# Performance work log

Measured on AMD Instinct MI355X. Metric: run time of the kernel, lower is better.

Reference implementation:

```python
import jax, jax.numpy as jnp
import numpy as np
from jax import lax

H = 20  # hidden_size


def _rnn_layer(x_seq, h0, W_ih, W_hh, b_ih, b_hh):
    """Vanilla tanh RNN layer. x_seq: [B,T,D], h0: [B,H]. Returns ([B,T,H], [B,H])."""
    # Precompute input projection for all timesteps (the only large GEMM).
    xp = jnp.einsum('btd,hd->bth', x_seq, W_ih) + b_ih + b_hh  # [B,T,H]

    def step(h, xt):
        h = jnp.tanh(xt + h @ W_hh.T)
        return h, h

    h_last, hs = lax.scan(step, h0, jnp.swapaxes(xp, 0, 1))  # hs: [T,B,H]
    return jnp.swapaxes(hs, 0, 1), h_last


def setup_inputs() -> dict:
    key = jax.random.key(0)
    ks = jax.random.split(key, 12)
    B, T = 4096, 512
    s = 1.0 / np.sqrt(H)  # PyTorch default uniform(-1/sqrt(H), 1/sqrt(H))
    u = lambda k, shape: jax.random.uniform(k, shape, jnp.float32, -s, s)
    return {
        'x': jax.random.normal(ks[0], (B, T, 1), jnp.float32),
        'hidden': jax.random.normal(ks[1], (2, B, H), jnp.float32),
        'W_ih0': u(ks[2], (H, 1)),
        'W_hh0': u(ks[3], (H, H)),
        'b_ih0': u(ks[4], (H,)),
        'b_hh0': u(ks[5], (H,)),
        'W_ih1': u(ks[6], (H, H)),
        'W_hh1': u(ks[7], (H, H)),
        'b_ih1': u(ks[8], (H,)),
        'b_hh1': u(ks[9], (H,)),
        'fc_w': u(ks[10], (1, H)),
        'fc_b': u(ks[11], (1,)),
    }


def reference(x, hidden, W_ih0, W_hh0, b_ih0, b_hh0, W_ih1, W_hh1, b_ih1, b_hh1, fc_w, fc_b):
    # 2-layer vanilla RNN (eval mode: inter-layer dropout disabled)
    h0_seq, h0_last = _rnn_layer(x, hidden[0], W_ih0, W_hh0, b_ih0, b_hh0)
    h1_seq, h1_last = _rnn_layer(h0_seq, hidden[1], W_ih1, W_hh1, b_ih1, b_hh1)
    out = h1_seq[:, -1, :] @ fc_w.T + fc_b  # [B,1]
    new_hidden = jnp.stack([h0_last, h1_last], axis=0)  # [2,B,H]
    return out, new_hidden
```

## Files before the change

### kernel.cpp

```cpp
#include <hip/hip_runtime.h>


#define Bsz 4096
#define Tn  512
#define Hn  20
#define GB  3
#define XPAD 520
#define NTHREADS 128

typedef float v2 __attribute__((ext_vector_type(2)));

__device__ __forceinline__ float tanh_fast(float v) {
    float e = __expf(2.0f * v);
    return 1.0f - 2.0f * __builtin_amdgcn_rcpf(e + 1.0f);
}

#define DOT20P(acc, accb, W, H) do { \
    acc  = __builtin_elementwise_fma(W##0, H##0, acc);  \
    accb = __builtin_elementwise_fma(W##1, H##1, accb); \
    acc  = __builtin_elementwise_fma(W##2, H##2, acc);  \
    accb = __builtin_elementwise_fma(W##3, H##3, accb); \
    acc  = __builtin_elementwise_fma(W##4, H##4, acc);  \
    accb = __builtin_elementwise_fma(W##5, H##5, accb); \
    acc  = __builtin_elementwise_fma(W##6, H##6, acc);  \
    accb = __builtin_elementwise_fma(W##7, H##7, accb); \
    acc  = __builtin_elementwise_fma(W##8, H##8, acc);  \
    accb = __builtin_elementwise_fma(W##9, H##9, accb); \
} while (0)

#define LOAD_ROWP(W, ptr) \
    v2 W##0, W##1, W##2, W##3, W##4, W##5, W##6, W##7, W##8, W##9; \
    { const float4* _p = (const float4*)(ptr); \
      float4 _t; \
      _t = _p[0]; W##0 = (v2){_t.x, _t.y}; W##1 = (v2){_t.z, _t.w}; \
      _t = _p[1]; W##2 = (v2){_t.x, _t.y}; W##3 = (v2){_t.z, _t.w}; \
      _t = _p[2]; W##4 = (v2){_t.x, _t.y}; W##5 = (v2){_t.z, _t.w}; \
      _t = _p[3]; W##6 = (v2){_t.x, _t.y}; W##7 = (v2){_t.z, _t.w}; \
      _t = _p[4]; W##8 = (v2){_t.x, _t.y}; W##9 = (v2){_t.z, _t.w}; }

#define READ_H(H, base) \
    v2 H##0, H##1, H##2, H##3, H##4, H##5, H##6, H##7, H##8, H##9; \
    { const float4 _a = *(const float4*)((base) + 0);  \
      const float4 _b = *(const float4*)((base) + 4);  \
      const float4 _c = *(const float4*)((base) + 8);  \
      const float4 _d = *(const float4*)((base) + 12); \
      const float4 _e = *(const float4*)((base) + 16); \
      H##0 = (v2){_a.x, _a.y}; H##1 = (v2){_a.z, _a.w}; \
      H##2 = (v2){_b.x, _b.y}; H##3 = (v2){_b.z, _b.w}; \
      H##4 = (v2){_c.x, _c.y}; H##5 = (v2){_c.z, _c.w}; \
      H##6 = (v2){_d.x, _d.y}; H##7 = (v2){_d.z, _d.w}; \
      H##8 = (v2){_e.x, _e.y}; H##9 = (v2){_e.z, _e.w}; }

__global__ __launch_bounds__(NTHREADS)
__attribute__((amdgpu_waves_per_eu(1, 4)))
void rnn2_fused(const float* __restrict__ x,
                const float* __restrict__ hidden,
                const float* __restrict__ W_ih0,
                const float* __restrict__ W_hh0,
                const float* __restrict__ b_ih0,
                const float* __restrict__ b_hh0,
                const float* __restrict__ W_ih1,
                const float* __restrict__ W_hh1,
                const float* __restrict__ b_ih1,
                const float* __restrict__ b_hh1,
                const float* __restrict__ fc_w,
                const float* __restrict__ fc_b,
                float* __restrict__ out)
{
    const int tid  = threadIdx.x;
    const int wave = tid >> 6;
    const int lane = tid & 63;
    int g = lane / Hn;
    int j = lane - g * Hn;
    const bool lane_ok = (lane < GB * Hn);
    if (!lane_ok) { g = GB - 1; j = lane - 60; }

    const int  b        = blockIdx.x * GB + g;
    const bool b_ok     = (b < Bsz);
    const int  bl       = b_ok ? b : (Bsz - 1);
    const bool store_ok = lane_ok && b_ok;

    __shared__ float xs[GB][XPAD];
    __shared__ float h0s[2][GB][Hn];
    __shared__ float h1s[GB][Hn];

    const float* rowA = (wave == 0) ? (W_hh0 + j * Hn) : (W_ih1 + j * Hn);
    LOAD_ROWP(wA, rowA)
    LOAD_ROWP(wB, W_hh1 + j * Hn)

    const float wih0  = W_ih0[j];
    const float bias0 = b_ih0[j] + b_hh0[j];
    const float bias1 = b_ih1[j] + b_hh1[j];

    {
        const int bB = blockIdx.x * GB;
        #pragma unroll
        for (int r = 0; r < (GB * Tn) / (NTHREADS * 4); ++r) {
            const int c  = (r * NTHREADS + tid) * 4;
            const int gg = c >> 9;
            const int t  = c & (Tn - 1);
            const int bb = (bB + gg < Bsz) ? (bB + gg) : (Bsz - 1);
            float4 v = *(const float4*)(x + (long)bb * Tn + t);
            *(float4*)&xs[gg][t] = v;
        }
    }

    if (wave == 0) h0s[1][g][j] = hidden[bl * Hn + j];
    else           h1s[g][j]    = hidden[(long)Bsz * Hn + bl * Hn + j];
    __syncthreads();

    float n_keep = 0.f;

    #pragma unroll 2
    for (int i = 0; i < Tn; ++i) {
        const int p = (i + 1) & 1, q = i & 1;
        if (wave == 0) {
            READ_H(hA, &h0s[p][g][0])
            const float xt = xs[g][i];
            v2 a  = (v2){fmaf(xt, wih0, bias0), 0.f};
            v2 ab = (v2){0.f, 0.f};
            DOT20P(a, ab, wA, hA);
            const v2 s = a + ab;
            const float n = tanh_fast(s.x + s.y);
            h0s[q][g][j] = n;
            n_keep = n;
        } else if (i > 0) {
            READ_H(hA, &h0s[p][g][0])
            READ_H(hB, &h1s[g][0])
            v2 a1  = (v2){bias1, 0.f};
            v2 a1b = (v2){0.f, 0.f};
            v2 a2  = (v2){0.f, 0.f};
            v2 a2b = (v2){0.f, 0.f};
            DOT20P(a1, a1b, wA, hA);
            DOT20P(a2, a2b, wB, hB);
            const v2 s = (a1 + a1b) + (a2 + a2b);
            const float n = tanh_fast(s.x + s.y);
            h1s[g][j] = n;
            n_keep = n;
        }
        __syncthreads();
    }

    if (wave == 0) {
        if (store_ok)
            out[Bsz + (long)b * Hn + j] = n_keep;
    } else {
        READ_H(hA, &h0s[1][g][0])
        READ_H(hB, &h1s[g][0])
        v2 a1  = (v2){bias1, 0.f};
        v2 a1b = (v2){0.f, 0.f};
        v2 a2  = (v2){0.f, 0.f};
        v2 a2b = (v2){0.f, 0.f};
        DOT20P(a1, a1b, wA, hA);
        DOT20P(a2, a2b, wB, hB);
        const v2 s = (a1 + a1b) + (a2 + a2b);
        const float n1_last = tanh_fast(s.x + s.y);
        h1s[g][j] = n1_last;

        if (store_ok) {
            out[Bsz + (long)Bsz * Hn + (long)b * Hn + j] = n1_last;
            if (j == 0) {
                LOAD_ROWP(fw, fc_w)
                READ_H(hv, &h1s[g][0])
                v2 aA = (v2){fc_b[0], 0.f};
                v2 aB = (v2){0.f, 0.f};
                DOT20P(aA, aB, fw, hv);
                const v2 sf = aA + aB;
                out[b] = sf.x + sf.y;
            }
        }
    }
}

extern "C" void kernel_launch(void* const* d_in, const int* in_sizes, int n_in,
                              void* d_out, int out_size, void* d_ws, size_t ws_size,
                              hipStream_t stream) {
    const float* x      = (const float*)d_in[0];
    const float* hidden = (const float*)d_in[1];
    const float* W_ih0  = (const float*)d_in[2];
    const float* W_hh0  = (const float*)d_in[3];
    const float* b_ih0  = (const float*)d_in[4];
    const float* b_hh0  = (const float*)d_in[5];
    const float* W_ih1  = (const float*)d_in[6];
    const float* W_hh1  = (const float*)d_in[7];
    const float* b_ih1  = (const float*)d_in[8];
    const float* b_hh1  = (const float*)d_in[9];
    const float* fc_w   = (const float*)d_in[10];
    const float* fc_b   = (const float*)d_in[11];

    const int nblocks = (Bsz + GB - 1) / GB;
    rnn2_fused<<<nblocks, NTHREADS, 0, stream>>>(
        x, hidden, W_ih0, W_hh0, b_ih0, b_hh0,
        W_ih1, W_hh1, b_ih1, b_hh1, fc_w, fc_b, (float*)d_out);
}
```

Measured before the change: 133.5 us.

## Pipeline RNN layers across waves with a ring buffer and fewer barriers

Replaces the per-timestep block barrier with phases of 8 timesteps. Wave 0 (layer 0) writes its hidden states into a 16-slot shared ring, and wave 1 (layer 1) runs one phase behind, reading the half of the ring that is already finished. Within each phase, each wave relies on in-wave LDS ordering for its own recurrence, which cuts block-wide barriers from one per step to one per phase. The cost is one extra phase of pipeline latency, a larger shared-memory ring, and reliance on intra-wavefront ordering of LDS accesses.

```diff
diff --git a/kernel.cpp b/kernel.cpp
--- a/kernel.cpp
+++ b/kernel.cpp
@@ -5,6 +5,9 @@
 #define Tn  512
 #define Hn  20
 #define GB  3
+#define K   8
+#define RING 16
+#define NPH (Tn / K)
 #define XPAD 520
 #define NTHREADS 128
 
@@ -81,7 +84,7 @@
     const bool store_ok = lane_ok && b_ok;
 
     __shared__ float xs[GB][XPAD];
-    __shared__ float h0s[2][GB][Hn];
+    __shared__ float h0r[RING][GB][Hn];
     __shared__ float h1s[GB][Hn];
 
     const float* rowA = (wave == 0) ? (W_hh0 + j * Hn) : (W_ih1 + j * Hn);
@@ -105,60 +108,58 @@
         }
     }
 
-    if (wave == 0) h0s[1][g][j] = hidden[bl * Hn + j];
-    else           h1s[g][j]    = hidden[(long)Bsz * Hn + bl * Hn + j];
+    if (wave == 0) h0r[RING - 1][g][j] = hidden[bl * Hn + j];
+    else           h1s[g][j]           = hidden[(long)Bsz * Hn + bl * Hn + j];
     __syncthreads();
 
     float n_keep = 0.f;
 
-    #pragma unroll 2
-    for (int i = 0; i < Tn; ++i) {
-        const int p = (i + 1) & 1, q = i & 1;
+    for (int k = 0; k <= NPH; ++k) {
         if (wave == 0) {
-            READ_H(hA, &h0s[p][g][0])
-            const float xt = xs[g][i];
-            v2 a  = (v2){fmaf(xt, wih0, bias0), 0.f};
-            v2 ab = (v2){0.f, 0.f};
-            DOT20P(a, ab, wA, hA);
-            const v2 s = a + ab;
-            const float n = tanh_fast(s.x + s.y);
-            h0s[q][g][j] = n;
-            n_keep = n;
-        } else if (i > 0) {
-            READ_H(hA, &h0s[p][g][0])
-            READ_H(hB, &h1s[g][0])
-            v2 a1  = (v2){bias1, 0.f};
-            v2 a1b = (v2){0.f, 0.f};
-            v2 a2  = (v2){0.f, 0.f};
-            v2 a2b = (v2){0.f, 0.f};
-            DOT20P(a1, a1b, wA, hA);
-            DOT20P(a2, a2b, wB, hB);
-            const v2 s = (a1 + a1b) + (a2 + a2b);
-            const float n = tanh_fast(s.x + s.y);
-            h1s[g][j] = n;
-            n_keep = n;
+            if (k < NPH) {
+                #pragma unroll
+                for (int u = 0; u < K; ++u) {
+                    const int t = k * K + u;
+                    READ_H(hA, &h0r[(t - 1) & (RING - 1)][g][0])
+                    const float xt = xs[g][t];
+                    v2 a  = (v2){fmaf(xt, wih0, bias0), 0.f};
+                    v2 ab = (v2){0.f, 0.f};
+                    DOT20P(a, ab, wA, hA);
+                    const v2 s = a + ab;
+                    const float n = tanh_fast(s.x + s.y);
+                    h0r[t & (RING - 1)][g][j] = n;
+                    n_keep = n;
+                }
+            }
+        } else {
+            if (k > 0) {
+                #pragma unroll
+                for (int u = 0; u < K; ++u) {
+                    const int t = (k - 1) * K + u;
+                    READ_H(hA, &h0r[t & (RING - 1)][g][0])
+                    READ_H(hB, &h1s[g][0])
+                    v2 a1  = (v2){bias1, 0.f};
+                    v2 a1b = (v2){0.f, 0.f};
+                    v2 a2  = (v2){0.f, 0.f};
+                    v2 a2b = (v2){0.f, 0.f};
+                    DOT20P(a1, a1b, wA, hA);
+                    DOT20P(a2, a2b, wB, hB);
+                    const v2 s = (a1 + a1b) + (a2 + a2b);
+                    const float n = tanh_fast(s.x + s.y);
+                    h1s[g][j] = n;
+                    n_keep = n;
+                }
+            }
         }
-        __syncthreads();
+        if (k < NPH) __syncthreads();
     }
 
     if (wave == 0) {
         if (store_ok)
             out[Bsz + (long)b * Hn + j] = n_keep;
     } else {
-        READ_H(hA, &h0s[1][g][0])
-        READ_H(hB, &h1s[g][0])
-        v2 a1  = (v2){bias1, 0.f};
-        v2 a1b = (v2){0.f, 0.f};
-        v2 a2  = (v2){0.f, 0.f};
-        v2 a2b = (v2){0.f, 0.f};
-        DOT20P(a1, a1b, wA, hA);
-        DOT20P(a2, a2b, wB, hB);
-        const v2 s = (a1 + a1b) + (a2 + a2b);
-        const float n1_last = tanh_fast(s.x + s.y);
-        h1s[g][j] = n1_last;
-
         if (store_ok) {
-            out[Bsz + (long)Bsz * Hn + (long)b * Hn + j] = n1_last;
+            out[Bsz + (long)Bsz * Hn + (long)b * Hn + j] = n_keep;
             if (j == 0) {
                 LOAD_ROWP(fw, fc_w)
                 READ_H(hv, &h1s[g][0])
```

Result: faster. 128.1 us (-4.0%).
